# Optimization experiments

Hardware: AMD Instinct MI355X
Metric: run time of the kernel (lower is better)

## Reference

```python
import jax, jax.numpy as jnp
import numpy as np

MARGIN = 0.3
BIG = 10000.0  # sentinel used by the original when a gt/lt negative set is empty


def setup_inputs() -> dict:
    key = jax.random.key(0)
    k1, k2 = jax.random.split(key)
    inputs = jax.random.normal(k1, (4096, 256), dtype=jnp.float32)
    targets = jax.random.randint(k2, (4096,), 0, 4, dtype=jnp.int32)
    return {"inputs": inputs, "targets": targets}


def reference(inputs, targets):
    # Pairwise Euclidean distance matrix (n, n).
    sq = jnp.sum(inputs * inputs, axis=1)
    d2 = sq[:, None] + sq[None, :] - 2.0 * (inputs @ inputs.T)
    dist = jnp.sqrt(jnp.maximum(d2, 0.0))

    # mask[i, j] semantics from the torch code (rows of expand are `targets`):
    #   eq: targets[j] == targets[i]; gt: targets[j] > targets[i]; lt: targets[j] < targets[i]
    eq = targets[None, :] == targets[:, None]
    gt = targets[None, :] > targets[:, None]
    lt = targets[None, :] < targets[:, None]

    # Hardest positive: max distance over same-label columns (diag always eq -> non-empty).
    hard_ap = jnp.max(jnp.where(eq, dist, -jnp.inf), axis=1)
    # Hardest greater / less negatives: min distance, sentinel BIG when set empty.
    an_g = jnp.min(jnp.where(gt, dist, jnp.inf), axis=1)
    an_g = jnp.where(jnp.isinf(an_g), BIG, an_g)
    an_l = jnp.min(jnp.where(lt, dist, jnp.inf), axis=1)
    an_l = jnp.where(jnp.isinf(an_l), BIG, an_l)

    loss = jnp.mean(jax.nn.relu(hard_ap - jnp.abs(an_g - an_l) + MARGIN))
    # cnt: rows whose positive set is just the anchor itself
    cnt = jnp.sum(jnp.sum(eq, axis=1) == 1)
    return loss, dist, cnt
```

## Files before the change

kernel.cpp:

```cpp
#include <hip/hip_runtime.h>

#define N 4096
#define D 256
#define MARGIN 0.3f
#define BIG 10000.0f

typedef _Float16 f16x8 __attribute__((ext_vector_type(8)));
typedef _Float16 f16x4 __attribute__((ext_vector_type(4)));
typedef float floatx16 __attribute__((ext_vector_type(16)));

__device__ inline void atomicMaxFloatPos(float* a, float v) {
    atomicMax((int*)a, __float_as_int(v));
}
__device__ inline void atomicMinFloatPos(float* a, float v) {
    atomicMin((int*)a, __float_as_int(v));
}

__device__ inline void gl_lds16(const void* g, void* l) {
    __builtin_amdgcn_global_load_lds(
        (const __attribute__((address_space(1))) unsigned int*)g,
        (__attribute__((address_space(3))) unsigned int*)l, 16, 0, 0);
}

__global__ __launch_bounds__(256) void prep_kernel(const float* __restrict__ x,
                                                   float* __restrict__ sq,
                                                   _Float16* __restrict__ Xf,
                                                   float* ap, float* ang, float* anl) {
    const int wave = threadIdx.x >> 6, lane = threadIdx.x & 63;
    const int row = blockIdx.x * 4 + wave;
    const float4 v = *(const float4*)(x + (size_t)row * D + lane * 4);
    f16x4 h;
    h[0] = (_Float16)v.x; h[1] = (_Float16)v.y;
    h[2] = (_Float16)v.z; h[3] = (_Float16)v.w;
    *(f16x4*)(Xf + (size_t)row * D + lane * 4) = h;
    const float c0 = (float)h[0], c1 = (float)h[1], c2 = (float)h[2], c3 = (float)h[3];
    float s = c0 * c0 + c1 * c1 + c2 * c2 + c3 * c3;
    #pragma unroll
    for (int off = 32; off; off >>= 1) s += __shfl_down(s, off);
    if (lane == 0) sq[row] = s;
    if (threadIdx.x < 4) {
        const int i = blockIdx.x * 4 + threadIdx.x;
        ap[i] = 0.0f; ang[i] = BIG; anl[i] = BIG;
    }
}

__global__ __launch_bounds__(64) void dist_kernel(const _Float16* __restrict__ Xf,
                                                  const int* __restrict__ tgt,
                                                  const float* __restrict__ sq,
                                                  float* __restrict__ dist,
                                                  float* ap, float* ang, float* anl) {
    __shared__ _Float16 lds[8192];
    _Float16* ldsA = lds;
    _Float16* ldsB = lds + 4096;
    float*    ldsC = (float*)lds;

    const int lane = threadIdx.x;
    const int row0 = blockIdx.y * 64;
    const int col0 = blockIdx.x * 64;

    const int drow = lane >> 3;
    const int q    = (lane & 7) ^ drow;

    floatx16 acc[2][2];
    #pragma unroll
    for (int mt = 0; mt < 2; ++mt)
        #pragma unroll
        for (int nt = 0; nt < 2; ++nt)
            #pragma unroll
            for (int r = 0; r < 16; ++r) acc[mt][nt][r] = 0.0f;

    const int m0 = lane & 31;
    const int m1 = 32 + m0;

    for (int s = 0; s < 4; ++s) {
        const int k0 = s * 64;
        __asm__ volatile("s_waitcnt lgkmcnt(0)" ::: "memory");
        #pragma unroll
        for (int d = 0; d < 8; ++d) {
            const int r = d * 8 + drow;
            gl_lds16(Xf + (size_t)(row0 + r) * D + k0 + q * 8, ldsA + d * 512);
            gl_lds16(Xf + (size_t)(col0 + r) * D + k0 + q * 8, ldsB + d * 512);
        }
        __asm__ volatile("s_waitcnt vmcnt(0)" ::: "memory");

        #pragma unroll
        for (int ks = 0; ks < 4; ++ks) {
            const int lq = ks * 2 + (lane >> 5);
            f16x8 a0 = *(const f16x8*)(ldsA + m0 * 64 + ((lq ^ (m0 & 7)) << 3));
            f16x8 a1 = *(const f16x8*)(ldsA + m1 * 64 + ((lq ^ (m1 & 7)) << 3));
            f16x8 b0 = *(const f16x8*)(ldsB + m0 * 64 + ((lq ^ (m0 & 7)) << 3));
            f16x8 b1 = *(const f16x8*)(ldsB + m1 * 64 + ((lq ^ (m1 & 7)) << 3));
            acc[0][0] = __builtin_amdgcn_mfma_f32_32x32x16_f16(a0, b0, acc[0][0], 0, 0, 0);
            acc[0][1] = __builtin_amdgcn_mfma_f32_32x32x16_f16(a0, b1, acc[0][1], 0, 0, 0);
            acc[1][0] = __builtin_amdgcn_mfma_f32_32x32x16_f16(a1, b0, acc[1][0], 0, 0, 0);
            acc[1][1] = __builtin_amdgcn_mfma_f32_32x32x16_f16(a1, b1, acc[1][1], 0, 0, 0);
        }
        __asm__ volatile("" ::: "memory");
    }

    const int gc0 = col0 + m0, gc1 = col0 + 32 + m0;
    const float sqc0 = sq[gc0], sqc1 = sq[gc1];
    const int rl_base = 4 * (lane >> 5);

    #pragma unroll
    for (int mt = 0; mt < 2; ++mt) {
        #pragma unroll
        for (int r = 0; r < 16; ++r) {
            const int row_l = mt * 32 + (r & 3) + 8 * (r >> 2) + rl_base;
            const int grow  = row0 + row_l;
            const float sqi = sq[grow];
            const float d0 = sqrtf(fmaxf(sqi + sqc0 - 2.0f * acc[mt][0][r], 0.0f));
            const float d1 = sqrtf(fmaxf(sqi + sqc1 - 2.0f * acc[mt][1][r], 0.0f));
            dist[(size_t)grow * N + gc0] = d0;
            dist[(size_t)grow * N + gc1] = d1;
            const int sw = row_l & 15;
            ldsC[row_l * 64 + (((m0 >> 2) ^ sw) << 2) + (m0 & 3)] = d0;
            ldsC[row_l * 64 + ((((m0 + 32) >> 2) ^ sw) << 2) + (m0 & 3)] = d1;
        }
    }
    __asm__ volatile("s_waitcnt lgkmcnt(0)" ::: "memory");

    const int grow = row0 + lane;
    const int ti   = tgt[grow];
    float mx = 0.0f, mg = BIG, ml = BIG;
    #pragma unroll
    for (int j = 0; j < 16; ++j) {
        const int4  t4 = *(const int4*)&tgt[col0 + j * 4];
        const float4 d4 = *(const float4*)&ldsC[lane * 64 + ((j ^ (lane & 15)) << 2)];
        if (t4.x == ti) mx = fmaxf(mx, d4.x); else if (t4.x > ti) mg = fminf(mg, d4.x); else ml = fminf(ml, d4.x);
        if (t4.y == ti) mx = fmaxf(mx, d4.y); else if (t4.y > ti) mg = fminf(mg, d4.y); else ml = fminf(ml, d4.y);
        if (t4.z == ti) mx = fmaxf(mx, d4.z); else if (t4.z > ti) mg = fminf(mg, d4.z); else ml = fminf(ml, d4.z);
        if (t4.w == ti) mx = fmaxf(mx, d4.w); else if (t4.w > ti) mg = fminf(mg, d4.w); else ml = fminf(ml, d4.w);
    }
    atomicMaxFloatPos(&ap[grow], mx);
    atomicMinFloatPos(&ang[grow], mg);
    atomicMinFloatPos(&anl[grow], ml);
}

__global__ __launch_bounds__(1024) void finish_kernel(const float* __restrict__ ap,
                                                      const float* __restrict__ ang,
                                                      const float* __restrict__ anl,
                                                      const int* __restrict__ tgt,
                                                      float* __restrict__ out) {
    __shared__ int hist[4];
    __shared__ unsigned hsum[2][16];
    __shared__ float wsum[16];
    __shared__ int wcnt[16];
    const int tid = threadIdx.x, lane = tid & 63, wv = tid >> 6;

    const int4 t4 = *(const int4*)&tgt[tid * 4];
    int c[4] = {0, 0, 0, 0};
    c[t4.x & 3]++; c[t4.y & 3]++; c[t4.z & 3]++; c[t4.w & 3]++;
    unsigned p01 = (unsigned)c[0] | ((unsigned)c[1] << 16);
    unsigned p23 = (unsigned)c[2] | ((unsigned)c[3] << 16);
    #pragma unroll
    for (int off = 32; off; off >>= 1) {
        p01 += __shfl_down(p01, off);
        p23 += __shfl_down(p23, off);
    }
    if (lane == 0) { hsum[0][wv] = p01; hsum[1][wv] = p23; }
    __syncthreads();
    if (tid == 0) {
        unsigned a = 0, b = 0;
        for (int i = 0; i < 16; ++i) { a += hsum[0][i]; b += hsum[1][i]; }
        hist[0] = a & 0xFFFF; hist[1] = a >> 16;
        hist[2] = b & 0xFFFF; hist[3] = b >> 16;
    }
    __syncthreads();

    float term = 0.0f; int cc = 0;
    const int lab[4] = {t4.x & 3, t4.y & 3, t4.z & 3, t4.w & 3};
    #pragma unroll
    for (int j = 0; j < 4; ++j) {
        const int i = tid * 4 + j;
        term += fmaxf(ap[i] - fabsf(ang[i] - anl[i]) + MARGIN, 0.0f);
        cc += (hist[lab[j]] == 1) ? 1 : 0;
    }
    #pragma unroll
    for (int off = 32; off; off >>= 1) {
        term += __shfl_down(term, off);
        cc   += __shfl_down(cc, off);
    }
    if (lane == 0) { wsum[wv] = term; wcnt[wv] = cc; }
    __syncthreads();
    if (tid == 0) {
        float ls = 0.0f; int cs = 0;
        for (int i = 0; i < 16; ++i) { ls += wsum[i]; cs += wcnt[i]; }
        out[0] = ls * (1.0f / N);
        out[1 + (size_t)N * N] = (float)cs;
    }
}

extern "C" void kernel_launch(void* const* d_in, const int* in_sizes, int n_in,
                              void* d_out, int out_size, void* d_ws, size_t ws_size,
                              hipStream_t stream) {
    const float* x   = (const float*)d_in[0];
    const int*   tgt = (const int*)d_in[1];
    float* out = (float*)d_out;
    char*  ws  = (char*)d_ws;

    _Float16* Xf  = (_Float16*)ws;
    float*    sq  = (float*)(ws + 2097152);
    float*    ap  = sq + 4096;
    float*    ang = sq + 8192;
    float*    anl = sq + 12288;

    prep_kernel<<<N / 4, 256, 0, stream>>>(x, sq, Xf, ap, ang, anl);
    dim3 grid(N / 64, N / 64);
    dist_kernel<<<grid, 64, 0, stream>>>(Xf, tgt, sq, out + 1, ap, ang, anl);
    finish_kernel<<<1, 1024, 0, stream>>>(ap, ang, anl, tgt, out);
}
```

Before: 115.1 us.

## Double-buffer K-stages of dist GEMM and use nontemporal dist stores

```diff
diff --git a/kernel.cpp b/kernel.cpp
--- a/kernel.cpp
+++ b/kernel.cpp
@@ -50,16 +50,14 @@
                                                   float* __restrict__ dist,
                                                   float* ap, float* ang, float* anl) {
     __shared__ _Float16 lds[8192];
-    _Float16* ldsA = lds;
-    _Float16* ldsB = lds + 4096;
-    float*    ldsC = (float*)lds;
+    float* ldsC = (float*)lds;
 
     const int lane = threadIdx.x;
     const int row0 = blockIdx.y * 64;
     const int col0 = blockIdx.x * 64;
 
-    const int drow = lane >> 3;
-    const int q    = (lane & 7) ^ drow;
+    const int drow = lane >> 2;
+    const int q    = (lane & 3) ^ (drow & 3);
 
     floatx16 acc[2][2];
     #pragma unroll
@@ -71,36 +69,57 @@
 
     const int m0 = lane & 31;
     const int m1 = 32 + m0;
-
-    for (int s = 0; s < 4; ++s) {
-        const int k0 = s * 64;
-        __asm__ volatile("s_waitcnt lgkmcnt(0)" ::: "memory");
+    const int hi = lane >> 5;
+    const int fsw = (m0 & 3);
+
+    #define ISSUE_STAGE(s)                                                            \
+    do {                                                                              \
+        _Float16* buf_ = lds + ((s) & 1) * 4096;                                      \
+        const int k0_ = (s) * 32;                                                     \
+        _Pragma("unroll")                                                             \
+        for (int d = 0; d < 4; ++d) {                                                 \
+            const int r_ = d * 16 + drow;                                             \
+            gl_lds16(Xf + (size_t)(row0 + r_) * D + k0_ + q * 8, buf_ + d * 512);     \
+            gl_lds16(Xf + (size_t)(col0 + r_) * D + k0_ + q * 8, buf_ + 2048 + d * 512); \
+        }                                                                             \
+    } while (0)
+
+    ISSUE_STAGE(0);
+    ISSUE_STAGE(1);
+
+    #pragma unroll
+    for (int s = 0; s < 8; ++s) {
+        if (s < 7) { __asm__ volatile("s_waitcnt vmcnt(8)" ::: "memory"); }
+        else       { __asm__ volatile("s_waitcnt vmcnt(0)" ::: "memory"); }
+
+        const _Float16* buf = lds + (s & 1) * 4096;
+        __builtin_amdgcn_s_setprio(1);
         #pragma unroll
-        for (int d = 0; d < 8; ++d) {
-            const int r = d * 8 + drow;
-            gl_lds16(Xf + (size_t)(row0 + r) * D + k0 + q * 8, ldsA + d * 512);
-            gl_lds16(Xf + (size_t)(col0 + r) * D + k0 + q * 8, ldsB + d * 512);
-        }
-        __asm__ volatile("s_waitcnt vmcnt(0)" ::: "memory");
-
-        #pragma unroll
-        for (int ks = 0; ks < 4; ++ks) {
-            const int lq = ks * 2 + (lane >> 5);
-            f16x8 a0 = *(const f16x8*)(ldsA + m0 * 64 + ((lq ^ (m0 & 7)) << 3));
-            f16x8 a1 = *(const f16x8*)(ldsA + m1 * 64 + ((lq ^ (m1 & 7)) << 3));
-            f16x8 b0 = *(const f16x8*)(ldsB + m0 * 64 + ((lq ^ (m0 & 7)) << 3));
-            f16x8 b1 = *(const f16x8*)(ldsB + m1 * 64 + ((lq ^ (m1 & 7)) << 3));
+        for (int ks = 0; ks < 2; ++ks) {
+            const int lq = ks * 2 + hi;
+            const int po = (lq ^ fsw) << 3;
+            f16x8 a0 = *(const f16x8*)(buf + m0 * 32 + po);
+            f16x8 a1 = *(const f16x8*)(buf + m1 * 32 + po);
+            f16x8 b0 = *(const f16x8*)(buf + 2048 + m0 * 32 + po);
+            f16x8 b1 = *(const f16x8*)(buf + 2048 + m1 * 32 + po);
             acc[0][0] = __builtin_amdgcn_mfma_f32_32x32x16_f16(a0, b0, acc[0][0], 0, 0, 0);
             acc[0][1] = __builtin_amdgcn_mfma_f32_32x32x16_f16(a0, b1, acc[0][1], 0, 0, 0);
             acc[1][0] = __builtin_amdgcn_mfma_f32_32x32x16_f16(a1, b0, acc[1][0], 0, 0, 0);
             acc[1][1] = __builtin_amdgcn_mfma_f32_32x32x16_f16(a1, b1, acc[1][1], 0, 0, 0);
         }
+        __builtin_amdgcn_s_setprio(0);
+
+        if (s < 6) {
+            __asm__ volatile("s_waitcnt lgkmcnt(0)" ::: "memory");
+            ISSUE_STAGE(s + 2);
+        }
         __asm__ volatile("" ::: "memory");
     }
+    #undef ISSUE_STAGE
 
     const int gc0 = col0 + m0, gc1 = col0 + 32 + m0;
     const float sqc0 = sq[gc0], sqc1 = sq[gc1];
-    const int rl_base = 4 * (lane >> 5);
+    const int rl_base = 4 * hi;
 
     #pragma unroll
     for (int mt = 0; mt < 2; ++mt) {
@@ -111,8 +130,8 @@
             const float sqi = sq[grow];
             const float d0 = sqrtf(fmaxf(sqi + sqc0 - 2.0f * acc[mt][0][r], 0.0f));
             const float d1 = sqrtf(fmaxf(sqi + sqc1 - 2.0f * acc[mt][1][r], 0.0f));
-            dist[(size_t)grow * N + gc0] = d0;
-            dist[(size_t)grow * N + gc1] = d1;
+            __builtin_nontemporal_store(d0, dist + (size_t)grow * N + gc0);
+            __builtin_nontemporal_store(d1, dist + (size_t)grow * N + gc1);
             const int sw = row_l & 15;
             ldsC[row_l * 64 + (((m0 >> 2) ^ sw) << 2) + (m0 & 3)] = d0;
             ldsC[row_l * 64 + ((((m0 + 32) >> 2) ^ sw) << 2) + (m0 & 3)] = d1;
```

Result: slower. 120.3 us (+4.5%).

## Fuse label reductions into the MFMA epilogue and halve the LDS tile size

Applied to the files above, without the earlier changes.

```diff
diff --git a/kernel.cpp b/kernel.cpp
--- a/kernel.cpp
+++ b/kernel.cpp
@@ -49,17 +49,16 @@
                                                   const float* __restrict__ sq,
                                                   float* __restrict__ dist,
                                                   float* ap, float* ang, float* anl) {
-    __shared__ _Float16 lds[8192];
-    _Float16* ldsA = lds;
-    _Float16* ldsB = lds + 4096;
-    float*    ldsC = (float*)lds;
+    __shared__ _Float16 lds[4096];
 
     const int lane = threadIdx.x;
     const int row0 = blockIdx.y * 64;
     const int col0 = blockIdx.x * 64;
 
-    const int drow = lane >> 3;
-    const int q    = (lane & 7) ^ drow;
+    const int g  = lane >> 3;
+    const int p  = lane & 7;
+    const int lq = p ^ g;
+    const _Float16* src0 = Xf + (size_t)((lq < 4 ? row0 : col0) + g) * D + (lq & 3) * 8;
 
     floatx16 acc[2][2];
     #pragma unroll
@@ -70,37 +69,45 @@
             for (int r = 0; r < 16; ++r) acc[mt][nt][r] = 0.0f;
 
     const int m0 = lane & 31;
-    const int m1 = 32 + m0;
-
-    for (int s = 0; s < 4; ++s) {
-        const int k0 = s * 64;
+    const int hi = lane >> 5;
+    const int sw = m0 & 7;
+
+    #pragma unroll
+    for (int s = 0; s < 8; ++s) {
+        const int k0 = s * 32;
         __asm__ volatile("s_waitcnt lgkmcnt(0)" ::: "memory");
         #pragma unroll
-        for (int d = 0; d < 8; ++d) {
-            const int r = d * 8 + drow;
-            gl_lds16(Xf + (size_t)(row0 + r) * D + k0 + q * 8, ldsA + d * 512);
-            gl_lds16(Xf + (size_t)(col0 + r) * D + k0 + q * 8, ldsB + d * 512);
-        }
+        for (int d = 0; d < 8; ++d)
+            gl_lds16(src0 + (size_t)d * 8 * D + k0, lds + d * 512);
         __asm__ volatile("s_waitcnt vmcnt(0)" ::: "memory");
 
-        #pragma unroll
-        for (int ks = 0; ks < 4; ++ks) {
-            const int lq = ks * 2 + (lane >> 5);
-            f16x8 a0 = *(const f16x8*)(ldsA + m0 * 64 + ((lq ^ (m0 & 7)) << 3));
-            f16x8 a1 = *(const f16x8*)(ldsA + m1 * 64 + ((lq ^ (m1 & 7)) << 3));
-            f16x8 b0 = *(const f16x8*)(ldsB + m0 * 64 + ((lq ^ (m0 & 7)) << 3));
-            f16x8 b1 = *(const f16x8*)(ldsB + m1 * 64 + ((lq ^ (m1 & 7)) << 3));
+        __builtin_amdgcn_s_setprio(1);
+        #pragma unroll
+        for (int ks = 0; ks < 2; ++ks) {
+            const int la = ks * 2 + hi;
+            f16x8 a0 = *(const f16x8*)(lds + m0 * 64        + ((la ^ sw) << 3));
+            f16x8 a1 = *(const f16x8*)(lds + (32 + m0) * 64 + ((la ^ sw) << 3));
+            f16x8 b0 = *(const f16x8*)(lds + m0 * 64        + (((4 + la) ^ sw) << 3));
+            f16x8 b1 = *(const f16x8*)(lds + (32 + m0) * 64 + (((4 + la) ^ sw) << 3));
             acc[0][0] = __builtin_amdgcn_mfma_f32_32x32x16_f16(a0, b0, acc[0][0], 0, 0, 0);
             acc[0][1] = __builtin_amdgcn_mfma_f32_32x32x16_f16(a0, b1, acc[0][1], 0, 0, 0);
             acc[1][0] = __builtin_amdgcn_mfma_f32_32x32x16_f16(a1, b0, acc[1][0], 0, 0, 0);
             acc[1][1] = __builtin_amdgcn_mfma_f32_32x32x16_f16(a1, b1, acc[1][1], 0, 0, 0);
         }
+        __builtin_amdgcn_s_setprio(0);
         __asm__ volatile("" ::: "memory");
     }
 
-    const int gc0 = col0 + m0, gc1 = col0 + 32 + m0;
+    const int tl = tgt[row0 + lane];
+    const unsigned long long pb0 = __ballot(tl & 1);
+    const unsigned long long pb1 = __ballot(tl & 2);
+    const int tc0 = tgt[col0 + m0], tc1 = tgt[col0 + 32 + m0];
+    const int gc0 = col0 + m0,      gc1 = col0 + 32 + m0;
     const float sqc0 = sq[gc0], sqc1 = sq[gc1];
-    const int rl_base = 4 * (lane >> 5);
+    const int rl_base = 4 * hi;
+
+    float mx0 = 0.0f, mg0 = BIG, ml0 = BIG;
+    float mx1 = 0.0f, mg1 = BIG, ml1 = BIG;
 
     #pragma unroll
     for (int mt = 0; mt < 2; ++mt) {
@@ -111,30 +118,32 @@
             const float sqi = sq[grow];
             const float d0 = sqrtf(fmaxf(sqi + sqc0 - 2.0f * acc[mt][0][r], 0.0f));
             const float d1 = sqrtf(fmaxf(sqi + sqc1 - 2.0f * acc[mt][1][r], 0.0f));
-            dist[(size_t)grow * N + gc0] = d0;
-            dist[(size_t)grow * N + gc1] = d1;
-            const int sw = row_l & 15;
-            ldsC[row_l * 64 + (((m0 >> 2) ^ sw) << 2) + (m0 & 3)] = d0;
-            ldsC[row_l * 64 + ((((m0 + 32) >> 2) ^ sw) << 2) + (m0 & 3)] = d1;
+            __builtin_nontemporal_store(d0, dist + (size_t)grow * N + gc0);
+            __builtin_nontemporal_store(d1, dist + (size_t)grow * N + gc1);
+            const int tr = (int)((pb0 >> row_l) & 1) | ((int)((pb1 >> row_l) & 1) << 1);
+            mx0 = fmaxf(mx0, (tr == tc0) ? d0 : 0.0f);
+            mg0 = fminf(mg0, (tr >  tc0) ? d0 : BIG);
+            ml0 = fminf(ml0, (tr <  tc0) ? d0 : BIG);
+            mx1 = fmaxf(mx1, (tr == tc1) ? d1 : 0.0f);
+            mg1 = fminf(mg1, (tr >  tc1) ? d1 : BIG);
+            ml1 = fminf(ml1, (tr <  tc1) ? d1 : BIG);
         }
     }
-    __asm__ volatile("s_waitcnt lgkmcnt(0)" ::: "memory");
-
-    const int grow = row0 + lane;
-    const int ti   = tgt[grow];
-    float mx = 0.0f, mg = BIG, ml = BIG;
-    #pragma unroll
-    for (int j = 0; j < 16; ++j) {
-        const int4  t4 = *(const int4*)&tgt[col0 + j * 4];
-        const float4 d4 = *(const float4*)&ldsC[lane * 64 + ((j ^ (lane & 15)) << 2)];
-        if (t4.x == ti) mx = fmaxf(mx, d4.x); else if (t4.x > ti) mg = fminf(mg, d4.x); else ml = fminf(ml, d4.x);
-        if (t4.y == ti) mx = fmaxf(mx, d4.y); else if (t4.y > ti) mg = fminf(mg, d4.y); else ml = fminf(ml, d4.y);
-        if (t4.z == ti) mx = fmaxf(mx, d4.z); else if (t4.z > ti) mg = fminf(mg, d4.z); else ml = fminf(ml, d4.z);
-        if (t4.w == ti) mx = fmaxf(mx, d4.w); else if (t4.w > ti) mg = fminf(mg, d4.w); else ml = fminf(ml, d4.w);
-    }
-    atomicMaxFloatPos(&ap[grow], mx);
-    atomicMinFloatPos(&ang[grow], mg);
-    atomicMinFloatPos(&anl[grow], ml);
+    mx0 = fmaxf(mx0, __shfl_xor(mx0, 32));
+    mg0 = fminf(mg0, __shfl_xor(mg0, 32));
+    ml0 = fminf(ml0, __shfl_xor(ml0, 32));
+    mx1 = fmaxf(mx1, __shfl_xor(mx1, 32));
+    mg1 = fminf(mg1, __shfl_xor(mg1, 32));
+    ml1 = fminf(ml1, __shfl_xor(ml1, 32));
+
+    if (hi == 0) {
+        atomicMaxFloatPos(&ap[gc0],  mx0);
+        atomicMinFloatPos(&ang[gc0], mg0);
+        atomicMinFloatPos(&anl[gc0], ml0);
+        atomicMaxFloatPos(&ap[gc1],  mx1);
+        atomicMinFloatPos(&ang[gc1], mg1);
+        atomicMinFloatPos(&anl[gc1], ml1);
+    }
 }
 
 __global__ __launch_bounds__(1024) void finish_kernel(const float* __restrict__ ap,
```

Result: slower. 120.2 us (+4.4%).
